# Kernel tuning notes

Hardware: AMD Instinct MI355X
Metric: run time of the kernel (lower is better)

Reference implementation:

```python
import jax, jax.numpy as jnp
import numpy as np

EPS = 1e-5
BETA = 1.0

def conv(x, w, stride, pad, b=None):
    y = jax.lax.conv_general_dilated(x, w, (stride, stride), ((pad, pad), (pad, pad)))
    if b is not None:
        y = y + b[None, :, None, None]
    return y

def conv_t(x, w, stride, pad, b=None):
    # torch ConvTranspose2d weight layout (Cin, Cout, kh, kw)
    wt = jnp.transpose(jnp.flip(w, (2, 3)), (1, 0, 2, 3))
    p = w.shape[2] - 1 - pad
    y = jax.lax.conv_general_dilated(x, wt, (1, 1), ((p, p), (p, p)), lhs_dilation=(stride, stride))
    if b is not None:
        y = y + b[None, :, None, None]
    return y

def bn(x, g, b):
    # training-mode BatchNorm2d over (B,H,W)
    m = jnp.mean(x, (0, 2, 3), keepdims=True)
    v = jnp.var(x, (0, 2, 3), keepdims=True)
    return (x - m) * jax.lax.rsqrt(v + EPS) * g[None, :, None, None] + b[None, :, None, None]

def resblock(x, w1, b1, w2, b2):
    h = conv(jax.nn.relu(x), w1, 1, 1, b1)   # 3x3
    h = conv(jax.nn.relu(h), w2, 1, 0, b2)   # 1x1
    return x + h

def quantize(z, emb):
    b_, c, h, w = z.shape
    flat = jnp.transpose(z, (0, 2, 3, 1)).reshape(-1, c)  # (N, code_dim)
    # squared euclidean distances; argmin matches cdist(p=2) argmin
    d2 = jnp.sum(flat * flat, 1, keepdims=True) - 2.0 * (flat @ emb.T) + jnp.sum(emb * emb, 1)[None, :]
    idxs = jnp.argmin(d2, axis=1)
    q = emb[idxs].reshape(b_, h, w, c).transpose(0, 3, 1, 2)
    return q, idxs.reshape(b_, h, w)

def setup_inputs() -> dict:
    key = jax.random.key(0)
    ks = jax.random.split(key, 32)
    C, CODE_SIZE = 64, 512
    def n(i, shape, s=0.05):
        return jax.random.normal(ks[i], shape, jnp.float32) * s
    inp = {
        'x': jax.random.normal(ks[0], (64, 3, 256, 256), jnp.float32),
        'c1_w': n(1, (C, 3, 4, 4)), 'c1_g': jnp.ones((C,), jnp.float32), 'c1_b': jnp.zeros((C,), jnp.float32),
        'c2_w': n(2, (C, C, 4, 4)), 'c2_g': jnp.ones((C,), jnp.float32), 'c2_b': jnp.zeros((C,), jnp.float32),
        'er1_w1': n(3, (C, C, 3, 3)), 'er1_b1': jnp.zeros((C,), jnp.float32),
        'er1_w2': n(4, (C, C, 1, 1)), 'er1_b2': jnp.zeros((C,), jnp.float32),
        'er2_w1': n(5, (C, C, 3, 3)), 'er2_b1': jnp.zeros((C,), jnp.float32),
        'er2_w2': n(6, (C, C, 1, 1)), 'er2_b2': jnp.zeros((C,), jnp.float32),
        'emb': jax.random.uniform(ks[7], (CODE_SIZE, C), jnp.float32, -1.0 / CODE_SIZE, 1.0 / CODE_SIZE),
        'dr1_w1': n(8, (C, C, 3, 3)), 'dr1_b1': jnp.zeros((C,), jnp.float32),
        'dr1_w2': n(9, (C, C, 1, 1)), 'dr1_b2': jnp.zeros((C,), jnp.float32),
        'dr2_w1': n(10, (C, C, 3, 3)), 'dr2_b1': jnp.zeros((C,), jnp.float32),
        'dr2_w2': n(11, (C, C, 1, 1)), 'dr2_b2': jnp.zeros((C,), jnp.float32),
        'dt1_w': n(12, (C, C, 4, 4)), 'dt1_g': jnp.ones((C,), jnp.float32), 'dt1_b': jnp.zeros((C,), jnp.float32),
        'dt2_w': n(13, (C, 3, 4, 4)), 'dt2_b': jnp.zeros((3,), jnp.float32),
    }
    return inp

def reference(x, c1_w, c1_g, c1_b, c2_w, c2_g, c2_b,
              er1_w1, er1_b1, er1_w2, er1_b2, er2_w1, er2_b1, er2_w2, er2_b2,
              emb,
              dr1_w1, dr1_b1, dr1_w2, dr1_b2, dr2_w1, dr2_b1, dr2_w2, dr2_b2,
              dt1_w, dt1_g, dt1_b, dt2_w, dt2_b):
    # encoder
    z = jax.nn.relu(bn(conv(x, c1_w, 2, 1), c1_g, c1_b))
    z = jax.nn.relu(bn(conv(z, c2_w, 2, 1), c2_g, c2_b))
    z = resblock(z, er1_w1, er1_b1, er1_w2, er1_b2)
    z = resblock(z, er2_w1, er2_b1, er2_w2, er2_b2)
    # vector quantization + straight-through
    q, idxs = quantize(z, emb)
    e_st = jax.lax.stop_gradient(q - z) + z
    # decoder
    d = resblock(e_st, dr1_w1, dr1_b1, dr1_w2, dr1_b2)
    d = resblock(d, dr2_w1, dr2_b1, dr2_w2, dr2_b2)
    d = jax.nn.relu(bn(conv_t(d, dt1_w, 2, 1), dt1_g, dt1_b))
    x_tilde = jnp.tanh(conv_t(d, dt2_w, 2, 1, dt2_b))
    vq_loss = jnp.mean((jax.lax.stop_gradient(z) - q) ** 2)
    commitment_loss = BETA * jnp.mean((jax.lax.stop_gradient(q) - z) ** 2)
    return (x_tilde, vq_loss, commitment_loss)
```

## Files before the change

kernel.cpp:

```cpp
#include <hip/hip_runtime.h>
#include <hip/hip_bf16.h>
#include <math.h>


#define NPOS   262144
#define OUTPIX 12582912

__device__ __forceinline__ void block_stats_atomic(double s, double q,
                                                   double* sum_p, double* sq_p) {
  #pragma unroll
  for (int o = 32; o; o >>= 1) { s += __shfl_down(s, o, 64); q += __shfl_down(q, o, 64); }
  __shared__ double ls[4], lq[4];
  int lane = threadIdx.x & 63, wv = threadIdx.x >> 6;
  if (lane == 0) { ls[wv] = s; lq[wv] = q; }
  __syncthreads();
  if (threadIdx.x == 0) {
    atomicAdd(sum_p, ls[0] + ls[1] + ls[2] + ls[3]);
    atomicAdd(sq_p,  lq[0] + lq[1] + lq[2] + lq[3]);
  }
}

__global__ void k_zero(double* p) { if (threadIdx.x < 385) p[threadIdx.x] = 0.0; }

__device__ __forceinline__ float np_pairwise64(const float* sq) {
  float r[8];
  #pragma unroll
  for (int j = 0; j < 8; j++) r[j] = sq[j];
  #pragma unroll
  for (int i = 8; i < 64; i += 8)
    #pragma unroll
    for (int j = 0; j < 8; j++) r[j] = __fadd_rn(r[j], sq[i + j]);
  return __fadd_rn(__fadd_rn(__fadd_rn(r[0], r[1]), __fadd_rn(r[2], r[3])),
                   __fadd_rn(__fadd_rn(r[4], r[5]), __fadd_rn(r[6], r[7])));
}

__global__ void k_ee(const float* __restrict__ emb, float* __restrict__ ee) {
  int e = blockIdx.x * 64 + threadIdx.x;
  const float* p = emb + e * 64;
  float sq[64];
  #pragma unroll
  for (int c = 0; c < 64; c++) sq[c] = __fmul_rn(p[c], p[c]);
  ee[e] = np_pairwise64(sq);
}

__global__ void k_finalize_bn(const double* __restrict__ sums, const double* __restrict__ sqs,
                              const float* __restrict__ g, const float* __restrict__ bt,
                              double* __restrict__ sc, double* __restrict__ sh, double invN) {
  int c = threadIdx.x;
  double m = sums[c] * invN;
  double var = sqs[c] * invN - m * m;
  double s = (double)g[c] / sqrt(var + 1e-5);
  sc[c] = s;
  sh[c] = (double)bt[c] - m * s;
}

__device__ __forceinline__ double conv1_acc(const float* __restrict__ x, const float* wr,
                                            int b, int oh, int ow) {
  double acc = 0.0;
  int ih0 = oh * 2 - 1, iw0 = ow * 2 - 1;
  for (int ic = 0; ic < 3; ic++) {
    const float* ip = x + (((long)(b * 3 + ic)) << 16);
    #pragma unroll
    for (int kh = 0; kh < 4; kh++) {
      int ih = ih0 + kh;
      if ((unsigned)ih < 256u) {
        const float* rp = ip + (ih << 8);
        #pragma unroll
        for (int kw = 0; kw < 4; kw++) {
          int iw = iw0 + kw;
          if ((unsigned)iw < 256u)
            acc += (double)rp[iw] * (double)wr[(ic * 4 + kh) * 4 + kw];
        }
      }
    }
  }
  return acc;
}

__global__ __launch_bounds__(256) void k_conv1_stats(const float* __restrict__ x,
                                                     const float* __restrict__ w,
                                                     double* __restrict__ stats) {
  int idx = blockIdx.x * 256 + threadIdx.x;
  int ow = idx & 127, oh = (idx >> 7) & 127, oc = (idx >> 14) & 63, b = idx >> 20;
  float wr[48];
  const float* wp = w + oc * 48;
  #pragma unroll
  for (int i = 0; i < 48; i++) wr[i] = wp[i];
  double acc = conv1_acc(x, wr, b, oh, ow);
  block_stats_atomic(acc, acc * acc, &stats[oc], &stats[64 + oc]);
}

__global__ __launch_bounds__(256) void k_conv1_store(const float* __restrict__ x,
                                                     const float* __restrict__ w,
                                                     const double* __restrict__ sc,
                                                     const double* __restrict__ sh,
                                                     double* __restrict__ a1s, int boff) {
  int idx = blockIdx.x * 256 + threadIdx.x;
  int ow = idx & 127, oh = (idx >> 7) & 127, oc = (idx >> 14) & 63, b = (idx >> 20) + boff;
  float wr[48];
  const float* wp = w + oc * 48;
  #pragma unroll
  for (int i = 0; i < 48; i++) wr[i] = wp[i];
  double acc = conv1_acc(x, wr, b, oh, ow);
  double v = acc * sc[oc] + sh[oc];
  a1s[idx] = v > 0.0 ? v : 0.0;
}

__global__ __launch_bounds__(256) void k_conv2(const double* __restrict__ in,
                                               const float* __restrict__ w,
                                               double* __restrict__ out,
                                               double* __restrict__ sum_p, double* __restrict__ sq_p) {
  int idx = blockIdx.x * 256 + threadIdx.x;
  int ow = idx & 63, oh = (idx >> 6) & 63, oc = (idx >> 12) & 63, bl = idx >> 18;
  __shared__ double wl[1024];
  const float* wp = w + oc * 1024;
  for (int i = threadIdx.x; i < 1024; i += 256) wl[i] = (double)wp[i];
  __syncthreads();
  double acc = 0.0;
  int ih0 = oh * 2 - 1, iw0 = ow * 2 - 1;
  for (int ic = 0; ic < 64; ic++) {
    const double* ip = in + (((long)(bl * 64 + ic)) << 14);
    const double* wc = &wl[ic * 16];
    #pragma unroll
    for (int kh = 0; kh < 4; kh++) {
      int ih = ih0 + kh;
      if ((unsigned)ih < 128u) {
        const double* rp = ip + (ih << 7);
        #pragma unroll
        for (int kw = 0; kw < 4; kw++) {
          int iw = iw0 + kw;
          if ((unsigned)iw < 128u) acc += rp[iw] * wc[kh * 4 + kw];
        }
      }
    }
  }
  out[idx] = acc;
  block_stats_atomic(acc, acc * acc, &sum_p[oc], &sq_p[oc]);
}

__global__ __launch_bounds__(256) void k_bn_apply(double* data, const double* __restrict__ sc,
                                                  const double* __restrict__ sh) {
  long idx = (long)blockIdx.x * 256 + threadIdx.x;
  int c = (int)((idx >> 12) & 63);
  double v = data[idx] * sc[c] + sh[c];
  data[idx] = v > 0.0 ? v : 0.0;
}

__global__ __launch_bounds__(256) void k_res3x3_d(const double* __restrict__ in,
                                                  const float* __restrict__ w,
                                                  const float* __restrict__ bias,
                                                  double* __restrict__ t) {
  int idx = blockIdx.x * 256 + threadIdx.x;
  int ow = idx & 63, oh = (idx >> 6) & 63, oc = (idx >> 12) & 63, bl = idx >> 18;
  __shared__ double wl[576];
  const float* wp = w + oc * 576;
  for (int i = threadIdx.x; i < 576; i += 256) wl[i] = (double)wp[i];
  __syncthreads();
  double acc = (double)bias[oc];
  for (int ic = 0; ic < 64; ic++) {
    const double* ip = in + (((long)(bl * 64 + ic)) << 12);
    const double* wc = &wl[ic * 9];
    #pragma unroll
    for (int kh = 0; kh < 3; kh++) {
      int ih = oh - 1 + kh;
      if ((unsigned)ih < 64u) {
        const double* rp = ip + (ih << 6);
        #pragma unroll
        for (int kw = 0; kw < 3; kw++) {
          int iw = ow - 1 + kw;
          if ((unsigned)iw < 64u) {
            double v = rp[iw];
            acc += (v > 0.0 ? v : 0.0) * wc[kh * 3 + kw];
          }
        }
      }
    }
  }
  t[idx] = acc;
}

__global__ __launch_bounds__(256) void k_res1x1_d(const double* __restrict__ t,
                                                  const float* __restrict__ w,
                                                  const float* __restrict__ bias,
                                                  double* __restrict__ x) {
  int idx = blockIdx.x * 256 + threadIdx.x;
  int p = idx & 4095, oc = (idx >> 12) & 63, bl = idx >> 18;
  __shared__ double wl[64];
  if (threadIdx.x < 64) wl[threadIdx.x] = (double)w[oc * 64 + threadIdx.x];
  __syncthreads();
  double acc = (double)bias[oc];
  const double* tp = t + (((long)bl) << 18) + p;
  for (int ic = 0; ic < 64; ic++) {
    double v = tp[(long)ic << 12];
    acc += (v > 0.0 ? v : 0.0) * wl[ic];
  }
  x[idx] = x[idx] + acc;
}

__global__ __launch_bounds__(256) void k_quant(double* __restrict__ z, const float* __restrict__ emb,
                                               const float* __restrict__ eesq,
                                               double* __restrict__ loss) {
  __shared__ float el[4096];
  __shared__ float ees[64];
  int n = blockIdx.x * 256 + threadIdx.x;
  int p = n & 4095, b = n >> 12;
  double* zp = z + (((long)b) << 18) + p;
  float z32[64];
  #pragma unroll
  for (int c = 0; c < 64; c++) z32[c] = (float)zp[(long)c << 12];
  float sq[64];
  #pragma unroll
  for (int c = 0; c < 64; c++) sq[c] = __fmul_rn(z32[c], z32[c]);
  float zz = np_pairwise64(sq);

  float best = 3.4e38f; int bi = 0;
  for (int e0 = 0; e0 < 512; e0 += 64) {
    __syncthreads();
    for (int i = threadIdx.x; i < 4096; i += 256) el[i] = emb[(e0 << 6) + i];
    if (threadIdx.x < 64) ees[threadIdx.x] = eesq[e0 + threadIdx.x];
    __syncthreads();
    for (int e = 0; e < 64; e++) {
      const float* ep = &el[e << 6];
      double dot = 0.0;
      #pragma unroll 8
      for (int c = 0; c < 64; c++) dot = fma((double)z32[c], (double)ep[c], dot);
      float t = __fmul_rn(2.0f, (float)dot);
      float d2 = __fadd_rn(__fsub_rn(zz, t), ees[e]);
      if (d2 < best) { best = d2; bi = e0 + e; }
    }
  }
  const float* ebp = emb + bi * 64;
  double l = 0.0;
  #pragma unroll
  for (int c = 0; c < 64; c++) {
    float ev = ebp[c];
    float est = __fadd_rn(__fsub_rn(ev, z32[c]), z32[c]);
    zp[(long)c << 12] = (double)est;
    float dd = __fsub_rn(z32[c], ev);
    l += (double)dd * (double)dd;
  }
  #pragma unroll
  for (int o = 32; o; o >>= 1) l += __shfl_down(l, o, 64);
  if ((threadIdx.x & 63) == 0) atomicAdd(loss, l);
}

__global__ __launch_bounds__(256) void k_res3x3_f(const double* __restrict__ in,
                                                  const float* __restrict__ w,
                                                  const float* __restrict__ bias,
                                                  float* __restrict__ t) {
  int idx = blockIdx.x * 256 + threadIdx.x;
  int ow = idx & 63, oh = (idx >> 6) & 63, oc = (idx >> 12) & 63, bl = idx >> 18;
  __shared__ float wl[576];
  const float* wp = w + oc * 576;
  for (int i = threadIdx.x; i < 576; i += 256) wl[i] = wp[i];
  __syncthreads();
  float acc = bias[oc];
  for (int ic = 0; ic < 64; ic++) {
    const double* ip = in + (((long)(bl * 64 + ic)) << 12);
    const float* wc = &wl[ic * 9];
    #pragma unroll
    for (int kh = 0; kh < 3; kh++) {
      int ih = oh - 1 + kh;
      if ((unsigned)ih < 64u) {
        const double* rp = ip + (ih << 6);
        #pragma unroll
        for (int kw = 0; kw < 3; kw++) {
          int iw = ow - 1 + kw;
          if ((unsigned)iw < 64u) acc += fmaxf((float)rp[iw], 0.f) * wc[kh * 3 + kw];
        }
      }
    }
  }
  t[idx] = acc;
}

__global__ __launch_bounds__(256) void k_res1x1_f(const float* __restrict__ t,
                                                  const float* __restrict__ w,
                                                  const float* __restrict__ bias,
                                                  double* __restrict__ x) {
  int idx = blockIdx.x * 256 + threadIdx.x;
  int p = idx & 4095, oc = (idx >> 12) & 63, bl = idx >> 18;
  __shared__ float wl[64];
  if (threadIdx.x < 64) wl[threadIdx.x] = w[oc * 64 + threadIdx.x];
  __syncthreads();
  float acc = bias[oc];
  const float* tp = t + (((long)bl) << 18) + p;
  for (int ic = 0; ic < 64; ic++) acc += fmaxf(tp[(long)ic << 12], 0.f) * wl[ic];
  x[idx] = (double)((float)x[idx] + acc);
}

__device__ __forceinline__ float convT1_acc(const double* __restrict__ in, const float* wl,
                                            int b, int oh, int ow) {
  int nh = 0, hih[2], hkh[2];
  for (int kh = (oh + 1) & 1; kh < 4; kh += 2) {
    int ih = (oh + 1 - kh) >> 1;
    if ((unsigned)ih < 64u) { hih[nh] = ih; hkh[nh] = kh; nh++; }
  }
  int nw = 0, wiw[2], wkw[2];
  for (int kw = (ow + 1) & 1; kw < 4; kw += 2) {
    int iw = (ow + 1 - kw) >> 1;
    if ((unsigned)iw < 64u) { wiw[nw] = iw; wkw[nw] = kw; nw++; }
  }
  float acc = 0.f;
  for (int ic = 0; ic < 64; ic++) {
    const double* ip = in + (((long)(b * 64 + ic)) << 12);
    const float* wc = &wl[ic << 4];
    for (int a = 0; a < nh; a++) {
      const double* rp = ip + (hih[a] << 6);
      int kb = hkh[a] << 2;
      for (int c2 = 0; c2 < nw; c2++) acc += (float)rp[wiw[c2]] * wc[kb + wkw[c2]];
    }
  }
  return acc;
}

__global__ __launch_bounds__(256) void k_convT1_stats(const double* __restrict__ in,
                                                      const float* __restrict__ w,
                                                      double* __restrict__ stats) {
  int idx = blockIdx.x * 256 + threadIdx.x;
  int ow = idx & 127, oh = (idx >> 7) & 127, oc = (idx >> 14) & 63, b = idx >> 20;
  __shared__ float wl[1024];
  for (int i = threadIdx.x; i < 1024; i += 256) {
    int ic = i >> 4, k = i & 15;
    wl[i] = w[(((long)ic * 64 + oc) << 4) + k];
  }
  __syncthreads();
  float acc = convT1_acc(in, wl, b, oh, ow);
  block_stats_atomic((double)acc, (double)acc * (double)acc, &stats[256 + oc], &stats[320 + oc]);
}

__global__ __launch_bounds__(256) void k_convT1_store(const double* __restrict__ in,
                                                      const float* __restrict__ w,
                                                      const double* __restrict__ sc,
                                                      const double* __restrict__ sh,
                                                      float* __restrict__ u, int boff) {
  int idx = blockIdx.x * 256 + threadIdx.x;
  int ow = idx & 127, oh = (idx >> 7) & 127, oc = (idx >> 14) & 63, b = (idx >> 20) + boff;
  __shared__ float wl[1024];
  for (int i = threadIdx.x; i < 1024; i += 256) {
    int ic = i >> 4, k = i & 15;
    wl[i] = w[(((long)ic * 64 + oc) << 4) + k];
  }
  __syncthreads();
  float acc = convT1_acc(in, wl, b, oh, ow);
  float v = acc * (float)sc[oc] + (float)sh[oc];
  u[idx] = fmaxf(v, 0.f);
}

__global__ __launch_bounds__(256) void k_convT2(const float* __restrict__ in,
                                                const float* __restrict__ w,
                                                const float* __restrict__ bias,
                                                float* __restrict__ out, long ooff) {
  int idx = blockIdx.x * 256 + threadIdx.x;
  int ow = idx & 255, oh = (idx >> 8) & 255;
  int t = idx >> 16;
  int oc = t % 3, bl = t / 3;
  __shared__ float wl[1024];
  for (int i = threadIdx.x; i < 1024; i += 256) {
    int ic = i >> 4, k = i & 15;
    wl[i] = w[(((long)ic * 3 + oc) << 4) + k];
  }
  __syncthreads();
  int nh = 0, hih[2], hkh[2];
  for (int kh = (oh + 1) & 1; kh < 4; kh += 2) {
    int ih = (oh + 1 - kh) >> 1;
    if ((unsigned)ih < 128u) { hih[nh] = ih; hkh[nh] = kh; nh++; }
  }
  int nw = 0, wiw[2], wkw[2];
  for (int kw = (ow + 1) & 1; kw < 4; kw += 2) {
    int iw = (ow + 1 - kw) >> 1;
    if ((unsigned)iw < 128u) { wiw[nw] = iw; wkw[nw] = kw; nw++; }
  }
  float acc = bias[oc];
  for (int ic = 0; ic < 64; ic++) {
    const float* ip = in + (((long)(bl * 64 + ic)) << 14);
    const float* wc = &wl[ic << 4];
    for (int a = 0; a < nh; a++) {
      const float* rp = ip + (hih[a] << 7);
      int kb = hkh[a] << 2;
      for (int c2 = 0; c2 < nw; c2++) acc += rp[wiw[c2]] * wc[kb + wkw[c2]];
    }
  }
  out[ooff + idx] = tanhf(acc);
}

__global__ void k_loss(const double* __restrict__ loss, float* __restrict__ out) {
  if (threadIdx.x == 0) {
    float m = (float)(loss[0] * (1.0 / 16777216.0));
    out[OUTPIX] = m;
    out[OUTPIX + 1] = m;
  }
}

extern "C" void kernel_launch(void* const* d_in, const int* in_sizes, int n_in,
                              void* d_out, int out_size, void* d_ws, size_t ws_size,
                              hipStream_t stream) {
  (void)in_sizes; (void)n_in; (void)out_size; (void)ws_size;
  const float* x      = (const float*)d_in[0];
  const float* c1_w   = (const float*)d_in[1];
  const float* c1_g   = (const float*)d_in[2];
  const float* c1_b   = (const float*)d_in[3];
  const float* c2_w   = (const float*)d_in[4];
  const float* c2_g   = (const float*)d_in[5];
  const float* c2_b   = (const float*)d_in[6];
  const float* er1_w1 = (const float*)d_in[7];
  const float* er1_b1 = (const float*)d_in[8];
  const float* er1_w2 = (const float*)d_in[9];
  const float* er1_b2 = (const float*)d_in[10];
  const float* er2_w1 = (const float*)d_in[11];
  const float* er2_b1 = (const float*)d_in[12];
  const float* er2_w2 = (const float*)d_in[13];
  const float* er2_b2 = (const float*)d_in[14];
  const float* emb    = (const float*)d_in[15];
  const float* dr1_w1 = (const float*)d_in[16];
  const float* dr1_b1 = (const float*)d_in[17];
  const float* dr1_w2 = (const float*)d_in[18];
  const float* dr1_b2 = (const float*)d_in[19];
  const float* dr2_w1 = (const float*)d_in[20];
  const float* dr2_b1 = (const float*)d_in[21];
  const float* dr2_w2 = (const float*)d_in[22];
  const float* dr2_b2 = (const float*)d_in[23];
  const float* dt1_w  = (const float*)d_in[24];
  const float* dt1_g  = (const float*)d_in[25];
  const float* dt1_b  = (const float*)d_in[26];
  const float* dt2_w  = (const float*)d_in[27];
  const float* dt2_b  = (const float*)d_in[28];
  float* out = (float*)d_out;

  char* ws = (char*)d_ws;
  double* stats = (double*)ws;
  double* bnp   = (double*)(ws + 3584);
  double* sc1 = bnp,       *sh1 = bnp + 64;
  double* sc2 = bnp + 128, *sh2 = bnp + 192;
  double* sc3 = bnp + 256, *sh3 = bnp + 320;
  float*  ee    = (float*)(ws + 8192);
  char* A = ws + 16384;
  double* Z64 = (double*)A;
  char*   SB  = A + 134217728;
  double* A1s  = (double*)SB;
  double* T64q = (double*)SB;
  float*  T32q = (float*)SB;
  float*  U32s = (float*)SB;

  const int GB_FULL1 = 67108864 / 256;
  const int GB_S1    = 4194304 / 256;
  const int GB_S2    = 1048576 / 256;
  const int GB_ZQ    = 4194304 / 256;
  const int GB_Z     = 16777216 / 256;
  const int GB_QU    = NPOS / 256;
  const int GB_O16   = 786432 / 256;

  k_zero<<<1, 512, 0, stream>>>(stats);
  k_ee<<<8, 64, 0, stream>>>(emb, ee);

  k_conv1_stats<<<GB_FULL1, 256, 0, stream>>>(x, c1_w, stats);
  k_finalize_bn<<<1, 64, 0, stream>>>(stats, stats + 64, c1_g, c1_b, sc1, sh1, 1.0 / 1048576.0);
  for (int s = 0; s < 16; s++) {
    k_conv1_store<<<GB_S1, 256, 0, stream>>>(x, c1_w, sc1, sh1, A1s, s * 4);
    k_conv2<<<GB_S2, 256, 0, stream>>>(A1s, c2_w, Z64 + (long)s * 1048576,
                                       stats + 128, stats + 192);
  }
  k_finalize_bn<<<1, 64, 0, stream>>>(stats + 128, stats + 192, c2_g, c2_b, sc2, sh2, 1.0 / 262144.0);
  k_bn_apply<<<GB_Z, 256, 0, stream>>>(Z64, sc2, sh2);

  for (int qr = 0; qr < 4; qr++) {
    double* zq = Z64 + (long)qr * 4194304;
    k_res3x3_d<<<GB_ZQ, 256, 0, stream>>>(zq, er1_w1, er1_b1, T64q);
    k_res1x1_d<<<GB_ZQ, 256, 0, stream>>>(T64q, er1_w2, er1_b2, zq);
  }
  for (int qr = 0; qr < 4; qr++) {
    double* zq = Z64 + (long)qr * 4194304;
    k_res3x3_d<<<GB_ZQ, 256, 0, stream>>>(zq, er2_w1, er2_b1, T64q);
    k_res1x1_d<<<GB_ZQ, 256, 0, stream>>>(T64q, er2_w2, er2_b2, zq);
  }

  k_quant<<<GB_QU, 256, 0, stream>>>(Z64, emb, ee, &stats[384]);

  for (int qr = 0; qr < 4; qr++) {
    double* sq = Z64 + (long)qr * 4194304;
    k_res3x3_f<<<GB_ZQ, 256, 0, stream>>>(sq, dr1_w1, dr1_b1, T32q);
    k_res1x1_f<<<GB_ZQ, 256, 0, stream>>>(T32q, dr1_w2, dr1_b2, sq);
  }
  for (int qr = 0; qr < 4; qr++) {
    double* sq = Z64 + (long)qr * 4194304;
    k_res3x3_f<<<GB_ZQ, 256, 0, stream>>>(sq, dr2_w1, dr2_b1, T32q);
    k_res1x1_f<<<GB_ZQ, 256, 0, stream>>>(T32q, dr2_w2, dr2_b2, sq);
  }

  k_convT1_stats<<<GB_FULL1, 256, 0, stream>>>(Z64, dt1_w, stats);
  k_finalize_bn<<<1, 64, 0, stream>>>(stats + 256, stats + 320, dt1_g, dt1_b, sc3, sh3, 1.0 / 1048576.0);
  for (int s = 0; s < 16; s++) {
    k_convT1_store<<<GB_S1, 256, 0, stream>>>(Z64, dt1_w, sc3, sh3, U32s, s * 4);
    k_convT2<<<GB_O16, 256, 0, stream>>>(U32s, dt2_w, dt2_b, out, (long)s * 786432);
  }

  k_loss<<<1, 64, 0, stream>>>(&stats[384], out);
}
```

Measured before the change: 55.52 ms.

## Store decoder activations as float in the double buffer and branchless transposed-conv taps

After quantization the decoder activations are written as float32 values into the even float slots of the existing double buffer. The decoder resblocks and the first transposed conv now read them as floats, which stops converting from double. Both transposed convs replace the data-dependent tap-list loops with a fixed four-tap, masked, unrolled formulation. The strided float layout still touches the same cache lines, so memory traffic barely changes, but the conversion work and branching go away.

Measured after the change: 47.42 ms. 14.6% less time.

```diff
diff --git a/kernel.cpp b/kernel.cpp
--- a/kernel.cpp
+++ b/kernel.cpp
@@ -230,12 +230,13 @@
     }
   }
   const float* ebp = emb + bi * 64;
+  float* fzp = (float*)zp;
   double l = 0.0;
   #pragma unroll
   for (int c = 0; c < 64; c++) {
     float ev = ebp[c];
     float est = __fadd_rn(__fsub_rn(ev, z32[c]), z32[c]);
-    zp[(long)c << 12] = (double)est;
+    fzp[(long)c << 13] = est;
     float dd = __fsub_rn(z32[c], ev);
     l += (double)dd * (double)dd;
   }
@@ -254,19 +255,20 @@
   const float* wp = w + oc * 576;
   for (int i = threadIdx.x; i < 576; i += 256) wl[i] = wp[i];
   __syncthreads();
+  const float* inf = (const float*)in;
   float acc = bias[oc];
   for (int ic = 0; ic < 64; ic++) {
-    const double* ip = in + (((long)(bl * 64 + ic)) << 12);
+    const float* ip = inf + (((long)(bl * 64 + ic)) << 13);
     const float* wc = &wl[ic * 9];
     #pragma unroll
     for (int kh = 0; kh < 3; kh++) {
       int ih = oh - 1 + kh;
       if ((unsigned)ih < 64u) {
-        const double* rp = ip + (ih << 6);
+        const float* rp = ip + (ih << 7);
         #pragma unroll
         for (int kw = 0; kw < 3; kw++) {
           int iw = ow - 1 + kw;
-          if ((unsigned)iw < 64u) acc += fmaxf((float)rp[iw], 0.f) * wc[kh * 3 + kw];
+          if ((unsigned)iw < 64u) acc += fmaxf(rp[iw << 1], 0.f) * wc[kh * 3 + kw];
         }
       }
     }
@@ -286,35 +288,39 @@
   float acc = bias[oc];
   const float* tp = t + (((long)bl) << 18) + p;
   for (int ic = 0; ic < 64; ic++) acc += fmaxf(tp[(long)ic << 12], 0.f) * wl[ic];
-  x[idx] = (double)((float)x[idx] + acc);
-}
-
-__device__ __forceinline__ float convT1_acc(const double* __restrict__ in, const float* wl,
+  float* xf = (float*)x;
+  long fi = (long)idx << 1;
+  xf[fi] = xf[fi] + acc;
+}
+
+__device__ __forceinline__ float convT1_acc(const float* __restrict__ inf, const float* wl,
                                             int b, int oh, int ow) {
-  int nh = 0, hih[2], hkh[2];
-  for (int kh = (oh + 1) & 1; kh < 4; kh += 2) {
-    int ih = (oh + 1 - kh) >> 1;
-    if ((unsigned)ih < 64u) { hih[nh] = ih; hkh[nh] = kh; nh++; }
-  }
-  int nw = 0, wiw[2], wkw[2];
-  for (int kw = (ow + 1) & 1; kw < 4; kw += 2) {
-    int iw = (ow + 1 - kw) >> 1;
-    if ((unsigned)iw < 64u) { wiw[nw] = iw; wkw[nw] = kw; nw++; }
-  }
+  int ph = (oh + 1) & 1, pw = (ow + 1) & 1;
+  int ih0 = (oh + 1 - ph) >> 1, iw0 = (ow + 1 - pw) >> 1;
+  int ih1 = ih0 - 1, iw1 = iw0 - 1;
+  bool vh0 = ih0 < 64, vh1 = ih1 >= 0, vw0 = iw0 < 64, vw1 = iw1 >= 0;
+  int ch0 = vh0 ? ih0 : 0, ch1 = vh1 ? ih1 : 0;
+  int cw0 = vw0 ? iw0 : 0, cw1 = vw1 ? iw1 : 0;
+  int o00 = (ch0 << 7) + (cw0 << 1), o01 = (ch0 << 7) + (cw1 << 1);
+  int o10 = (ch1 << 7) + (cw0 << 1), o11 = (ch1 << 7) + (cw1 << 1);
+  bool m00 = vh0 && vw0, m01 = vh0 && vw1, m10 = vh1 && vw0, m11 = vh1 && vw1;
+  int wA = ph * 4 + pw, wB = wA + 2, wC = wA + 8, wD = wA + 10;
   float acc = 0.f;
+  const float* ip = inf + (((long)b) << 19);
+  #pragma unroll 8
   for (int ic = 0; ic < 64; ic++) {
-    const double* ip = in + (((long)(b * 64 + ic)) << 12);
+    const float* pp = ip + ((long)ic << 13);
     const float* wc = &wl[ic << 4];
-    for (int a = 0; a < nh; a++) {
-      const double* rp = ip + (hih[a] << 6);
-      int kb = hkh[a] << 2;
-      for (int c2 = 0; c2 < nw; c2++) acc += (float)rp[wiw[c2]] * wc[kb + wkw[c2]];
-    }
+    float v00 = m00 ? pp[o00] : 0.f;
+    float v01 = m01 ? pp[o01] : 0.f;
+    float v10 = m10 ? pp[o10] : 0.f;
+    float v11 = m11 ? pp[o11] : 0.f;
+    acc += v00 * wc[wA] + v01 * wc[wB] + v10 * wc[wC] + v11 * wc[wD];
   }
   return acc;
 }
 
-__global__ __launch_bounds__(256) void k_convT1_stats(const double* __restrict__ in,
+__global__ __launch_bounds__(256) void k_convT1_stats(const float* __restrict__ inf,
                                                       const float* __restrict__ w,
                                                       double* __restrict__ stats) {
   int idx = blockIdx.x * 256 + threadIdx.x;
@@ -325,11 +331,11 @@
     wl[i] = w[(((long)ic * 64 + oc) << 4) + k];
   }
   __syncthreads();
-  float acc = convT1_acc(in, wl, b, oh, ow);
+  float acc = convT1_acc(inf, wl, b, oh, ow);
   block_stats_atomic((double)acc, (double)acc * (double)acc, &stats[256 + oc], &stats[320 + oc]);
 }
 
-__global__ __launch_bounds__(256) void k_convT1_store(const double* __restrict__ in,
+__global__ __launch_bounds__(256) void k_convT1_store(const float* __restrict__ inf,
                                                       const float* __restrict__ w,
                                                       const double* __restrict__ sc,
                                                       const double* __restrict__ sh,
@@ -342,7 +348,7 @@
     wl[i] = w[(((long)ic * 64 + oc) << 4) + k];
   }
   __syncthreads();
-  float acc = convT1_acc(in, wl, b, oh, ow);
+  float acc = convT1_acc(inf, wl, b, oh, ow);
   float v = acc * (float)sc[oc] + (float)sh[oc];
   u[idx] = fmaxf(v, 0.f);
 }
@@ -361,25 +367,27 @@
     wl[i] = w[(((long)ic * 3 + oc) << 4) + k];
   }
   __syncthreads();
-  int nh = 0, hih[2], hkh[2];
-  for (int kh = (oh + 1) & 1; kh < 4; kh += 2) {
-    int ih = (oh + 1 - kh) >> 1;
-    if ((unsigned)ih < 128u) { hih[nh] = ih; hkh[nh] = kh; nh++; }
-  }
-  int nw = 0, wiw[2], wkw[2];
-  for (int kw = (ow + 1) & 1; kw < 4; kw += 2) {
-    int iw = (ow + 1 - kw) >> 1;
-    if ((unsigned)iw < 128u) { wiw[nw] = iw; wkw[nw] = kw; nw++; }
-  }
+  int ph = (oh + 1) & 1, pw = (ow + 1) & 1;
+  int ih0 = (oh + 1 - ph) >> 1, iw0 = (ow + 1 - pw) >> 1;
+  int ih1 = ih0 - 1, iw1 = iw0 - 1;
+  bool vh0 = ih0 < 128, vh1 = ih1 >= 0, vw0 = iw0 < 128, vw1 = iw1 >= 0;
+  int ch0 = vh0 ? ih0 : 0, ch1 = vh1 ? ih1 : 0;
+  int cw0 = vw0 ? iw0 : 0, cw1 = vw1 ? iw1 : 0;
+  int o00 = (ch0 << 7) + cw0, o01 = (ch0 << 7) + cw1;
+  int o10 = (ch1 << 7) + cw0, o11 = (ch1 << 7) + cw1;
+  bool m00 = vh0 && vw0, m01 = vh0 && vw1, m10 = vh1 && vw0, m11 = vh1 && vw1;
+  int wA = ph * 4 + pw, wB = wA + 2, wC = wA + 8, wD = wA + 10;
   float acc = bias[oc];
+  const float* ip = in + (((long)bl) << 20);
+  #pragma unroll 8
   for (int ic = 0; ic < 64; ic++) {
-    const float* ip = in + (((long)(bl * 64 + ic)) << 14);
+    const float* pp = ip + ((long)ic << 14);
     const float* wc = &wl[ic << 4];
-    for (int a = 0; a < nh; a++) {
-      const float* rp = ip + (hih[a] << 7);
-      int kb = hkh[a] << 2;
-      for (int c2 = 0; c2 < nw; c2++) acc += rp[wiw[c2]] * wc[kb + wkw[c2]];
-    }
+    float v00 = m00 ? pp[o00] : 0.f;
+    float v01 = m01 ? pp[o01] : 0.f;
+    float v10 = m10 ? pp[o10] : 0.f;
+    float v11 = m11 ? pp[o11] : 0.f;
+    acc += v00 * wc[wA] + v01 * wc[wB] + v10 * wc[wC] + v11 * wc[wD];
   }
   out[ooff + idx] = tanhf(acc);
 }
@@ -487,10 +495,10 @@
     k_res1x1_f<<<GB_ZQ, 256, 0, stream>>>(T32q, dr2_w2, dr2_b2, sq);
   }
 
-  k_convT1_stats<<<GB_FULL1, 256, 0, stream>>>(Z64, dt1_w, stats);
+  k_convT1_stats<<<GB_FULL1, 256, 0, stream>>>((const float*)Z64, dt1_w, stats);
   k_finalize_bn<<<1, 64, 0, stream>>>(stats + 256, stats + 320, dt1_g, dt1_b, sc3, sh3, 1.0 / 1048576.0);
   for (int s = 0; s < 16; s++) {
-    k_convT1_store<<<GB_S1, 256, 0, stream>>>(Z64, dt1_w, sc3, sh3, U32s, s * 4);
+    k_convT1_store<<<GB_S1, 256, 0, stream>>>((const float*)Z64, dt1_w, sc3, sh3, U32s, s * 4);
     k_convT2<<<GB_O16, 256, 0, stream>>>(U32s, dt2_w, dt2_b, out, (long)s * 786432);
   }
 
```
